# Kernel tuning notes

Hardware: AMD Instinct MI355X
Metric: run time of the kernel (lower is better)

## Reference

```python
import jax, jax.numpy as jnp
import numpy as np


def setup_inputs() -> dict:
    key = jax.random.key(0)
    k1, k2, k3 = jax.random.split(key, 3)
    N, C_in, H, W = 32, 16, 256, 256
    C_out, K = 64, 3
    x = jax.random.normal(k1, (N, C_in, H, W), dtype=jnp.float32)
    # match nn.Conv2d default init scale roughly (values irrelevant for correctness harness)
    fan_in = C_in * K * K
    bound = 1.0 / np.sqrt(fan_in)
    conv_weight = jax.random.normal(k2, (C_out, C_in, K, K), dtype=jnp.float32) * bound
    conv_bias = jax.random.normal(k3, (C_out,), dtype=jnp.float32) * bound
    return {"x": x, "conv_weight": conv_weight, "conv_bias": conv_bias}


def reference(x, conv_weight, conv_bias):
    # Conv2d: stride=1, padding=0 (VALID), dilation=1, groups=1
    y = jax.lax.conv_general_dilated(
        x, conv_weight,
        window_strides=(1, 1), padding='VALID',
        dimension_numbers=('NCHW', 'OIHW', 'NCHW'),
    ) + conv_bias[None, :, None, None]          # (N, C_out, OH, OW)
    y = jnp.min(y, axis=1, keepdims=True)       # min over output channels -> (N, 1, OH, OW)
    return jnp.tanh(jnp.tanh(y))                # double tanh
```

## Files before the change

### kernel.cpp

```cpp
#include <hip/hip_runtime.h>
#include <hip/hip_bf16.h>

typedef __attribute__((ext_vector_type(8)))  short short8;
typedef __attribute__((ext_vector_type(4)))  float f32x4;
typedef __attribute__((ext_vector_type(16))) float f32x16;

#define CIN   16
#define HH    256
#define WW    256
#define OHH   254
#define OWW   254
#define HW    (HH * WW)

#define SLOTU  (36 * 8)
#define HALF_R (16 * SLOTU + 8)

__device__ __forceinline__ ushort f2bf(float f) {
    unsigned u = __builtin_bit_cast(unsigned, f);
    unsigned r = (u + 0x7fffu + ((u >> 16) & 1u)) >> 16;
    return (ushort)r;
}

__device__ __forceinline__ float dtanh2(float x) {
    const float K = 2.8853900817779268f;
    float xc = fminf(fmaxf(x, -9.0f), 9.0f);
    float e1 = __builtin_amdgcn_exp2f(K * xc);
    float t1 = 1.0f - 2.0f * __builtin_amdgcn_rcpf(e1 + 1.0f);
    float e2 = __builtin_amdgcn_exp2f(K * t1);
    return 1.0f - 2.0f * __builtin_amdgcn_rcpf(e2 + 1.0f);
}

__device__ __forceinline__ float rmin16(f32x16 a) {
    float t0 = fminf(fminf(a[0],  a[1]),  fminf(a[2],  a[3]));
    float t1 = fminf(fminf(a[4],  a[5]),  fminf(a[6],  a[7]));
    float t2 = fminf(fminf(a[8],  a[9]),  fminf(a[10], a[11]));
    float t3 = fminf(fminf(a[12], a[13]), fminf(a[14], a[15]));
    return fminf(fminf(t0, t1), fminf(t2, t3));
}

__global__ void prep_weights(const float* __restrict__ wsrc, ushort* __restrict__ wfrag) {
    int idx = blockIdx.x * 256 + threadIdx.x;
    if (idx >= 9216) return;
    int r    = idx & 7;
    int lane = (idx >> 3) & 63;
    int j    = (idx >> 9) & 1;
    int tap  = idx >> 10;
    int ci   = 8 * (lane >> 5) + r;
    int co   = j * 32 + (lane & 31);
    int kh   = tap / 3, kw = tap - 3 * kh;
    wfrag[idx] = f2bf(wsrc[(co * CIN + ci) * 9 + kh * 3 + kw]);
}

__global__ __launch_bounds__(256, 3) void conv_min_tanh(
        const float* __restrict__ x, const ushort* __restrict__ wfrag,
        const float* __restrict__ bias, float* __restrict__ out) {
    __shared__ ushort ring[2 * HALF_R];
    __shared__ ushort mp[2][2][4][32];

    const int tid   = threadIdx.x;
    const int ow0   = blockIdx.x * 32;
    const int hbase = blockIdx.y * 64;
    const int n     = blockIdx.z;
    const float* xb = x + (size_t)n * CIN * HW;

    auto stage_inline = [&](int pos) {
        int lr_  = pos / 36;
        int rm_  = pos - lr_ * 36;
        int ciq_ = rm_ / 9;
        int w4_  = rm_ - ciq_ * 9;
        int hg  = min(hbase + lr_, HH - 1);
        int wg_ = min(ow0 + 4 * w4_, WW - 4);
        const float* src = xb + (size_t)(ciq_ * 4) * HW + hg * WW + wg_;
        f32x4 v0 = *reinterpret_cast<const f32x4*>(src);
        f32x4 v1 = *reinterpret_cast<const f32x4*>(src + HW);
        f32x4 v2 = *reinterpret_cast<const f32x4*>(src + 2 * HW);
        f32x4 v3 = *reinterpret_cast<const f32x4*>(src + 3 * HW);
        ushort* dst = &ring[(ciq_ >> 1) * HALF_R + lr_ * SLOTU + (4 * w4_) * 8 + (ciq_ & 1) * 4];
#pragma unroll
        for (int e = 0; e < 4; ++e) {
            unsigned lo, hi;
            asm("v_cvt_pk_bf16_f32 %0, %1, %2" : "=v"(lo) : "v"(v0[e]), "v"(v1[e]));
            asm("v_cvt_pk_bf16_f32 %0, %1, %2" : "=v"(hi) : "v"(v2[e]), "v"(v3[e]));
            uint2 pk; pk.x = lo; pk.y = hi;
            *reinterpret_cast<uint2*>(dst + e * 8) = pk;
        }
    };
    stage_inline(tid);
    if (tid < 32) stage_inline(tid + 256);

    const bool sa = (tid < 144);
    const int lr  = tid / 36;
    const int rm  = tid - lr * 36;
    const int ciq = rm / 9;
    const int w4  = rm - ciq * 9;
    const int wg  = min(ow0 + 4 * w4, WW - 4);
    const float* gbase = xb + (size_t)(ciq * 4) * HW + wg;
    ushort* sdst = &ring[(ciq >> 1) * HALF_R + (4 * w4) * 8 + (ciq & 1) * 4];

    f32x4 ra0 = {}, ra1 = {}, ra2 = {}, ra3 = {};
    f32x4 rb0 = {}, rb1 = {}, rb2 = {}, rb3 = {};

#define ISSUE(cc, r0, r1, r2, r3)                                              \
    if (sa) {                                                                  \
        int hg = min(hbase + 4 * (cc) + lr, HH - 1);                           \
        const float* s_ = gbase + hg * WW;                                     \
        asm volatile("global_load_dwordx4 %0, %1, off" : "=v"(r0) : "v"(s_) : "memory");           \
        asm volatile("global_load_dwordx4 %0, %1, off" : "=v"(r1) : "v"(s_ + HW) : "memory");      \
        asm volatile("global_load_dwordx4 %0, %1, off" : "=v"(r2) : "v"(s_ + 2 * HW) : "memory");  \
        asm volatile("global_load_dwordx4 %0, %1, off" : "=v"(r3) : "v"(s_ + 3 * HW) : "memory");  \
    }

#define WRITEBK(cc, r0, r1, r2, r3)                                            \
    if (sa) {                                                                  \
        ushort* d_ = sdst + ((4 * (cc) + lr) & 15) * SLOTU;                    \
        _Pragma("unroll")                                                      \
        for (int e = 0; e < 4; ++e) {                                          \
            unsigned lo_, hi_;                                                 \
            asm("v_cvt_pk_bf16_f32 %0, %1, %2" : "=v"(lo_) : "v"(r0[e]), "v"(r1[e]));  \
            asm("v_cvt_pk_bf16_f32 %0, %1, %2" : "=v"(hi_) : "v"(r2[e]), "v"(r3[e]));  \
            uint2 pk_; pk_.x = lo_; pk_.y = hi_;                               \
            *reinterpret_cast<uint2*>(d_ + e * 8) = pk_;                       \
        }                                                                      \
    }

    ISSUE(2, ra0, ra1, ra2, ra3);
    ISSUE(3, rb0, rb1, rb2, rb3);

    const int lane  = tid & 63;
    const int wid   = tid >> 6;
    const int jw    = wid & 1;
    const int rq    = wid >> 1;
    const int px    = lane & 31;
    const int khalf = lane >> 5;
    short8 wf[9];
#pragma unroll
    for (int tap = 0; tap < 9; ++tap)
        wf[tap] = *reinterpret_cast<const short8*>(wfrag + ((tap * 2 + jw) * 64 + lane) * 8);
    f32x16 bi;
#pragma unroll
    for (int q4 = 0; q4 < 4; ++q4) {
        f32x4 b = *reinterpret_cast<const f32x4*>(bias + jw * 32 + 4 * khalf + 8 * q4);
#pragma unroll
        for (int s = 0; s < 4; ++s) bi[q4 * 4 + s] = b[s];
    }
    const ushort* bptr = &ring[khalf * HALF_R + px * 8];

    asm volatile("s_waitcnt lgkmcnt(0)" ::: "memory");
    __builtin_amdgcn_s_barrier();

#pragma unroll 2
    for (int c = 0; c < 16; ++c) {
        {
            const int R0 = 4 * c + 2 * rq;
            f32x16 a0 = bi, a1 = bi;
#pragma unroll
            for (int t = 0; t < 4; ++t) {
                const ushort* rp = bptr + ((R0 + t) & 15) * SLOTU;
                short8 f0 = *reinterpret_cast<const short8*>(rp);
                short8 f1 = *reinterpret_cast<const short8*>(rp + 8);
                short8 f2 = *reinterpret_cast<const short8*>(rp + 16);
                if (t < 3) {
                    a0 = __builtin_amdgcn_mfma_f32_32x32x16_bf16(wf[t * 3 + 0], f0, a0, 0, 0, 0);
                    a0 = __builtin_amdgcn_mfma_f32_32x32x16_bf16(wf[t * 3 + 1], f1, a0, 0, 0, 0);
                    a0 = __builtin_amdgcn_mfma_f32_32x32x16_bf16(wf[t * 3 + 2], f2, a0, 0, 0, 0);
                }
                if (t >= 1) {
                    a1 = __builtin_amdgcn_mfma_f32_32x32x16_bf16(wf[(t - 1) * 3 + 0], f0, a1, 0, 0, 0);
                    a1 = __builtin_amdgcn_mfma_f32_32x32x16_bf16(wf[(t - 1) * 3 + 1], f1, a1, 0, 0, 0);
                    a1 = __builtin_amdgcn_mfma_f32_32x32x16_bf16(wf[(t - 1) * 3 + 2], f2, a1, 0, 0, 0);
                }
            }
            float v0 = rmin16(a0), v1 = rmin16(a1);
            v0 = fminf(v0, __shfl_xor(v0, 32, 64));
            v1 = fminf(v1, __shfl_xor(v1, 32, 64));
            if (lane < 32) {
                mp[c & 1][jw][2 * rq + 0][px] = f2bf(v0);
                mp[c & 1][jw][2 * rq + 1][px] = f2bf(v1);
            }
        }

        if (c < 15) {
            if ((c & 1) == 0) {
                asm volatile("s_waitcnt vmcnt(4)"
                             : "+v"(ra0), "+v"(ra1), "+v"(ra2), "+v"(ra3) :: "memory");
                WRITEBK(c + 2, ra0, ra1, ra2, ra3);
                ISSUE(min(c + 4, 16), ra0, ra1, ra2, ra3);
            } else {
                asm volatile("s_waitcnt vmcnt(4)"
                             : "+v"(rb0), "+v"(rb1), "+v"(rb2), "+v"(rb3) :: "memory");
                WRITEBK(c + 2, rb0, rb1, rb2, rb3);
                ISSUE(min(c + 4, 16), rb0, rb1, rb2, rb3);
            }
        }

        asm volatile("s_waitcnt lgkmcnt(0)" ::: "memory");
        __builtin_amdgcn_s_barrier();

        if (tid < 128) {
            const int r4 = tid >> 5, opx = tid & 31;
            float f0 = __builtin_bit_cast(float, (unsigned)mp[c & 1][0][r4][opx] << 16);
            float f1 = __builtin_bit_cast(float, (unsigned)mp[c & 1][1][r4][opx] << 16);
            float y  = dtanh2(fminf(f0, f1));
            const int oh = hbase + 4 * c + r4;
            const int ow = ow0 + opx;
            if (oh < OHH && ow < OWW)
                out[((size_t)n * OHH + oh) * OWW + ow] = y;
        }
    }
#undef ISSUE
#undef WRITEBK
}

extern "C" void kernel_launch(void* const* d_in, const int* in_sizes, int n_in,
                              void* d_out, int out_size, void* d_ws, size_t ws_size,
                              hipStream_t stream) {
    const float* x = (const float*)d_in[0];
    const float* w = (const float*)d_in[1];
    const float* b = (const float*)d_in[2];
    float* out     = (float*)d_out;
    ushort* wfrag  = (ushort*)d_ws;

    prep_weights<<<36, 256, 0, stream>>>(w, wfrag);
    dim3 grid(8, 4, 32);
    conv_min_tanh<<<grid, dim3(256, 1, 1), 0, stream>>>(x, wfrag, b, out);
}
```

Measured before the change: 56.18 us.

## Cut prefetch depth to one register set and raise occupancy to four blocks

Replaces the two-deep register prefetch of input rows (ra/rb alternating, vmcnt(4)) with a single register set that is waited to completion before writeback, and raises the launch bound minimum from 3 to 4 blocks per CU. The aim is to free VGPRs so more waves fit per CU and hide memory latency through occupancy instead of a deeper software pipeline. In exchange each iteration now waits on its load fully with only one iteration of lookahead, which can expose global-load latency.

Measured after the change: 53.47 us. 4.8% less time.

```diff
diff --git a/kernel.cpp b/kernel.cpp
--- a/kernel.cpp
+++ b/kernel.cpp
@@ -51,7 +51,7 @@
     wfrag[idx] = f2bf(wsrc[(co * CIN + ci) * 9 + kh * 3 + kw]);
 }
 
-__global__ __launch_bounds__(256, 3) void conv_min_tanh(
+__global__ __launch_bounds__(256, 4) void conv_min_tanh(
         const float* __restrict__ x, const ushort* __restrict__ wfrag,
         const float* __restrict__ bias, float* __restrict__ out) {
     __shared__ ushort ring[2 * HALF_R];
@@ -98,33 +98,31 @@
     ushort* sdst = &ring[(ciq >> 1) * HALF_R + (4 * w4) * 8 + (ciq & 1) * 4];
 
     f32x4 ra0 = {}, ra1 = {}, ra2 = {}, ra3 = {};
-    f32x4 rb0 = {}, rb1 = {}, rb2 = {}, rb3 = {};
-
-#define ISSUE(cc, r0, r1, r2, r3)                                              \
+
+#define ISSUE(cc)                                                              \
     if (sa) {                                                                  \
         int hg = min(hbase + 4 * (cc) + lr, HH - 1);                           \
         const float* s_ = gbase + hg * WW;                                     \
-        asm volatile("global_load_dwordx4 %0, %1, off" : "=v"(r0) : "v"(s_) : "memory");           \
-        asm volatile("global_load_dwordx4 %0, %1, off" : "=v"(r1) : "v"(s_ + HW) : "memory");      \
-        asm volatile("global_load_dwordx4 %0, %1, off" : "=v"(r2) : "v"(s_ + 2 * HW) : "memory");  \
-        asm volatile("global_load_dwordx4 %0, %1, off" : "=v"(r3) : "v"(s_ + 3 * HW) : "memory");  \
-    }
-
-#define WRITEBK(cc, r0, r1, r2, r3)                                            \
+        asm volatile("global_load_dwordx4 %0, %1, off" : "=v"(ra0) : "v"(s_) : "memory");           \
+        asm volatile("global_load_dwordx4 %0, %1, off" : "=v"(ra1) : "v"(s_ + HW) : "memory");      \
+        asm volatile("global_load_dwordx4 %0, %1, off" : "=v"(ra2) : "v"(s_ + 2 * HW) : "memory");  \
+        asm volatile("global_load_dwordx4 %0, %1, off" : "=v"(ra3) : "v"(s_ + 3 * HW) : "memory");  \
+    }
+
+#define WRITEBK(cc)                                                            \
     if (sa) {                                                                  \
         ushort* d_ = sdst + ((4 * (cc) + lr) & 15) * SLOTU;                    \
         _Pragma("unroll")                                                      \
         for (int e = 0; e < 4; ++e) {                                          \
             unsigned lo_, hi_;                                                 \
-            asm("v_cvt_pk_bf16_f32 %0, %1, %2" : "=v"(lo_) : "v"(r0[e]), "v"(r1[e]));  \
-            asm("v_cvt_pk_bf16_f32 %0, %1, %2" : "=v"(hi_) : "v"(r2[e]), "v"(r3[e]));  \
+            asm("v_cvt_pk_bf16_f32 %0, %1, %2" : "=v"(lo_) : "v"(ra0[e]), "v"(ra1[e]));  \
+            asm("v_cvt_pk_bf16_f32 %0, %1, %2" : "=v"(hi_) : "v"(ra2[e]), "v"(ra3[e]));  \
             uint2 pk_; pk_.x = lo_; pk_.y = hi_;                               \
             *reinterpret_cast<uint2*>(d_ + e * 8) = pk_;                       \
         }                                                                      \
     }
 
-    ISSUE(2, ra0, ra1, ra2, ra3);
-    ISSUE(3, rb0, rb1, rb2, rb3);
+    ISSUE(2);
 
     const int lane  = tid & 63;
     const int wid   = tid >> 6;
@@ -180,17 +178,10 @@
         }
 
         if (c < 15) {
-            if ((c & 1) == 0) {
-                asm volatile("s_waitcnt vmcnt(4)"
-                             : "+v"(ra0), "+v"(ra1), "+v"(ra2), "+v"(ra3) :: "memory");
-                WRITEBK(c + 2, ra0, ra1, ra2, ra3);
-                ISSUE(min(c + 4, 16), ra0, ra1, ra2, ra3);
-            } else {
-                asm volatile("s_waitcnt vmcnt(4)"
-                             : "+v"(rb0), "+v"(rb1), "+v"(rb2), "+v"(rb3) :: "memory");
-                WRITEBK(c + 2, rb0, rb1, rb2, rb3);
-                ISSUE(min(c + 4, 16), rb0, rb1, rb2, rb3);
-            }
+            asm volatile("s_waitcnt vmcnt(0)"
+                         : "+v"(ra0), "+v"(ra1), "+v"(ra2), "+v"(ra3) :: "memory");
+            WRITEBK(c + 2);
+            ISSUE(min(c + 3, 16));
         }
 
         asm volatile("s_waitcnt lgkmcnt(0)" ::: "memory");
```
